# Performance work log

Measured on AMD Instinct MI355X. Metric: run time of the kernel, lower is better.

## Reference

```python
import jax, jax.numpy as jnp
import numpy as np

LN_EPS = 1e-5


def _segment_mean(vals, idx, num_segments):
    s = jax.ops.segment_sum(vals, idx, num_segments=num_segments)
    cnt = jax.ops.segment_sum(jnp.ones((vals.shape[0],), vals.dtype), idx, num_segments=num_segments)
    return s / jnp.maximum(cnt, 1.0)[:, None]


def _sage_layer(x, src, dst, W_l, b_l, W_r, gamma, beta):
    # PyG SAGEConv (mean aggr): out = lin_l(mean_{j in N(i)} x_j) + lin_r(x_i)
    N = x.shape[0]
    agg = _segment_mean(x[src], dst, N)                     # [N, in]
    h = agg @ W_l.T + b_l + x @ W_r.T                       # [N, out]
    mu = jnp.mean(h, axis=-1, keepdims=True)
    var = jnp.mean((h - mu) ** 2, axis=-1, keepdims=True)
    h = (h - mu) * jax.lax.rsqrt(var + LN_EPS) * gamma + beta
    return jax.nn.relu(h)                                   # dropout: eval mode (identity)


def setup_inputs() -> dict:
    key = jax.random.key(0)
    ks = jax.random.split(key, 20)
    N, E, IN, H, OUT, G, C = 50000, 600000, 128, 128, 64, 64, 2

    def glorot(k, fo, fi):
        lim = np.sqrt(6.0 / (fo + fi)).astype(np.float32)
        return jax.random.uniform(k, (fo, fi), jnp.float32, -lim, lim)

    inp = {
        'x': jax.random.normal(ks[0], (N, IN), jnp.float32),
        'edge_index': jax.random.randint(ks[1], (2, E), 0, N, jnp.int64),
        'batch': jnp.sort(jax.random.randint(ks[2], (N,), 0, G, jnp.int64)),
    }
    dims = [(IN, H), (H, H), (H, OUT)]
    for i, (fi, fo) in enumerate(dims):
        inp[f'Wl{i}'] = glorot(ks[3 + 4 * i], fo, fi)
        inp[f'bl{i}'] = jnp.zeros((fo,), jnp.float32)
        inp[f'Wr{i}'] = glorot(ks[4 + 4 * i], fo, fi)
        inp[f'g{i}'] = jnp.ones((fo,), jnp.float32)
        inp[f'be{i}'] = jnp.zeros((fo,), jnp.float32)
    inp['cW1'] = glorot(ks[16], H, 2 * OUT)
    inp['cb1'] = jnp.zeros((H,), jnp.float32)
    inp['cW2'] = glorot(ks[17], C, H)
    inp['cb2'] = jnp.zeros((C,), jnp.float32)
    return inp


def reference(x, edge_index, batch,
              Wl0, bl0, Wr0, g0, be0,
              Wl1, bl1, Wr1, g1, be1,
              Wl2, bl2, Wr2, g2, be2,
              cW1, cb1, cW2, cb2):
    src, dst = edge_index[0], edge_index[1]
    h = _sage_layer(x, src, dst, Wl0, bl0, Wr0, g0, be0)
    h = _sage_layer(h, src, dst, Wl1, bl1, Wr1, g1, be1)
    h = _sage_layer(h, src, dst, Wl2, bl2, Wr2, g2, be2)
    G = 64  # number of graphs
    x_mean = _segment_mean(h, batch, G)                     # [G, out]
    x_max = jax.ops.segment_max(h, batch, num_segments=G)   # [G, out]
    z = jnp.concatenate([x_mean, x_max], axis=-1)           # [G, 2*out]
    z = jax.nn.relu(z @ cW1.T + cb1)
    return z @ cW2.T + cb2                                  # [G, num_classes]
```

## Files before the change

kernel.cpp:

```cpp
#include <hip/hip_runtime.h>

typedef unsigned short ushort_t;
typedef short s16x8 __attribute__((ext_vector_type(8)));
typedef float f32x4 __attribute__((ext_vector_type(4)));

#define LN_EPS 1e-5f

__device__ __forceinline__ float b2f(ushort_t u) {
    return __uint_as_float(((unsigned)u) << 16);
}
__device__ __forceinline__ ushort_t f2b(float f) {
    unsigned b = __float_as_uint(f);
    b += 0x7FFFu + ((b >> 16) & 1u);
    return (ushort_t)(b >> 16);
}
__device__ __forceinline__ unsigned f2b2(float lo, float hi) {
    return (unsigned)f2b(lo) | ((unsigned)f2b(hi) << 16);
}
__device__ __forceinline__ float ldf(const void* p, size_t i, int isF) {
    return isF ? ((const float*)p)[i] : b2f(((const ushort_t*)p)[i]);
}

__global__ void GraphSAGE_36026185678961_kernel() {}

__global__ void k_detect_zero(const void* w0, const void* ei, int* __restrict__ flags,
                              int* __restrict__ deg, float* __restrict__ Z, int N) {
    int i = blockIdx.x * blockDim.x + threadIdx.x;
    if (i < N) deg[i] = 0;
    if (i < 64 * 128) Z[i] = 0.f;
    if (blockIdx.x == 0 && threadIdx.x < 64) {
        int t = threadIdx.x;
        const ushort_t* u = (const ushort_t*)w0;
        int pass = 0;
        #pragma unroll
        for (int k = 0; k < 4; ++k) {
            ushort_t v = u[t * 4 + k];
            int ex = (v >> 7) & 0xFF;
            if (ex == 0 || (ex >= 0x60 && ex <= 0x7E)) pass++;
        }
        const unsigned* w = (const unsigned*)ei;
        int nz = (w[2 * t + 1] != 0u) ? 1 : 0;
        #pragma unroll
        for (int off = 32; off; off >>= 1) {
            pass += __shfl_down(pass, off, 64);
            nz += __shfl_down(nz, off, 64);
        }
        if (t == 0) {
            flags[0] = (pass < 205) ? 1 : 0;
            flags[1] = (nz == 0) ? 1 : 0;
        }
    }
}

__global__ void k_prep(const void* X, ushort_t* __restrict__ XB, int total4, int xb,
                       const void* ei, int E, int N, int* __restrict__ deg, int eb,
                       const void* Wl0, const void* Wr0, const void* Wl1, const void* Wr1,
                       const void* Wl2, const void* Wr2,
                       ushort_t* __restrict__ Wb0, ushort_t* __restrict__ Wb1,
                       ushort_t* __restrict__ Wb2,
                       const int* __restrict__ flags) {
    int b = blockIdx.x;
    if (b < xb) {
        int idx = b * 256 + threadIdx.x;
        if (idx >= total4) return;
        if (flags[0]) {
            float4 v = ((const float4*)X)[idx];
            ushort4 o;
            o.x = f2b(v.x); o.y = f2b(v.y); o.z = f2b(v.z); o.w = f2b(v.w);
            ((ushort4*)XB)[idx] = o;
        } else {
            ((ushort4*)XB)[idx] = ((const ushort4*)X)[idx];
        }
    } else if (b < xb + eb) {
        int e = (b - xb) * 256 + threadIdx.x;
        if (e >= E) return;
        int d = flags[1] ? (int)((const long long*)ei)[E + e] : ((const int*)ei)[E + e];
        if ((unsigned)d < (unsigned)N) atomicAdd(&deg[d], 1);
    } else {
        int t = (b - xb - eb) * 256 + threadIdx.x;
        int isF = flags[0];
        if (t < 2 * 32768) {
            const void* Wl = (t < 32768) ? Wl0 : Wl1;
            const void* Wr = (t < 32768) ? Wr0 : Wr1;
            ushort_t* Wb = (t < 32768) ? Wb0 : Wb1;
            int base = t & 32767;
            int f = base >> 8, k = base & 255;
            if (isF) {
                float v = (k < 128) ? ((const float*)Wl)[f * 128 + k]
                                    : ((const float*)Wr)[f * 128 + (k - 128)];
                Wb[base] = f2b(v);
            } else {
                Wb[base] = ((const ushort_t*)((k < 128) ? Wl : Wr))[f * 128 + (k & 127)];
            }
        } else if (t < 2 * 32768 + 16384) {
            int base = t - 2 * 32768;
            int f = base >> 7, k = base & 127;
            const void* W = (f < 64) ? Wl2 : Wr2;
            int fr = f & 63;
            Wb2[base] = isF ? f2b(((const float*)W)[fr * 128 + k])
                            : ((const ushort_t*)W)[fr * 128 + k];
        }
    }
}

__global__ void k_scan1(const int* __restrict__ deg, int N,
                        int* __restrict__ rowptr, int* __restrict__ bsum) {
    __shared__ int wsum[4];
    __shared__ int wpre[4];
    int tid = threadIdx.x;
    int lane = tid & 63;
    int w = tid >> 6;
    int i = blockIdx.x * 256 + tid;
    int v = (i < N) ? deg[i] : 0;
    int x = v;
    #pragma unroll
    for (int off = 1; off < 64; off <<= 1) {
        int t = __shfl_up(x, off, 64);
        if (lane >= off) x += t;
    }
    if (lane == 63) wsum[w] = x;
    __syncthreads();
    if (tid == 0) {
        int a = wsum[0]; wpre[0] = a;
        a += wsum[1]; wpre[1] = a;
        a += wsum[2]; wpre[2] = a;
        a += wsum[3]; wpre[3] = a;
    }
    __syncthreads();
    int woff = (w == 0) ? 0 : wpre[w - 1];
    if (i < N) rowptr[i] = woff + x - v;
    if (tid == 0) bsum[blockIdx.x] = wpre[3];
}

__global__ void k_scan2(const int* __restrict__ bsum, int nb,
                        int* __restrict__ boff, int* __restrict__ rowptrN,
                        const void* batch, int N, int G, const int* __restrict__ flags,
                        int* __restrict__ bounds) {
    __shared__ int wsum[4];
    __shared__ int wpre[4];
    int tid = threadIdx.x;
    int lane = tid & 63;
    int w = tid >> 6;
    int run = 0;
    for (int base = 0; base < nb; base += 256) {
        int i = base + tid;
        int v = (i < nb) ? bsum[i] : 0;
        int x = v;
        #pragma unroll
        for (int off = 1; off < 64; off <<= 1) {
            int t = __shfl_up(x, off, 64);
            if (lane >= off) x += t;
        }
        if (lane == 63) wsum[w] = x;
        __syncthreads();
        if (tid == 0) {
            int a = wsum[0]; wpre[0] = a;
            a += wsum[1]; wpre[1] = a;
            a += wsum[2]; wpre[2] = a;
            a += wsum[3]; wpre[3] = a;
        }
        __syncthreads();
        int woff = (w == 0) ? 0 : wpre[w - 1];
        if (i < nb) boff[i] = run + woff + x - v;
        int tot = wpre[3];
        __syncthreads();
        run += tot;
    }
    if (tid == 0) *rowptrN = run;
    if (tid <= G) {
        int isL = flags[1];
        int lo = 0, hi = N;
        while (lo < hi) {
            int mid = (lo + hi) >> 1;
            int bv = isL ? (int)((const long long*)batch)[mid] : ((const int*)batch)[mid];
            if (bv < tid) lo = mid + 1; else hi = mid;
        }
        bounds[tid] = lo;
    }
}

__global__ void k_scan3(int* __restrict__ rowptr, const int* __restrict__ boff,
                        int* __restrict__ cursor, int N) {
    int i = blockIdx.x * 256 + threadIdx.x;
    if (i < N) {
        int r = rowptr[i] + boff[i >> 8];
        rowptr[i] = r;
        cursor[i] = r;
    }
}

__global__ void k_fill(const void* ei, int E, int N, const int* __restrict__ flags,
                       int* __restrict__ cursor, int* __restrict__ col) {
    int e = blockIdx.x * blockDim.x + threadIdx.x;
    if (e >= E) return;
    int s, d;
    if (flags[1]) {
        const long long* p = (const long long*)ei;
        s = (int)p[e];
        d = (int)p[E + e];
    } else {
        const int* p = (const int*)ei;
        s = p[e];
        d = p[E + e];
    }
    if ((unsigned)d < (unsigned)N) {
        int p = atomicAdd(&cursor[d], 1);
        if ((unsigned)p < (unsigned)E) col[p] = ((unsigned)s < (unsigned)N) ? s : 0;
    }
}

__global__ __launch_bounds__(256) void k_agg(
    const ushort_t* __restrict__ X, const int* __restrict__ rowptr,
    const int* __restrict__ col, ushort_t* __restrict__ AGG, int N) {
    int i = blockIdx.x * 4 + (threadIdx.x >> 6);
    if (i >= N) return;
    int l = threadIdx.x & 63;
    int qn = l >> 4;
    int fo = l & 15;
    const uint4* X8 = (const uint4*)X;
    int s = rowptr[i], e = rowptr[i + 1];
    float al[4] = {0.f, 0.f, 0.f, 0.f};
    float ah[4] = {0.f, 0.f, 0.f, 0.f};
    int p = s + qn;
    for (; p + 8 < e; p += 12) {
        int j0 = col[p], j1 = col[p + 4], j2 = col[p + 8];
        uint4 u0 = X8[(size_t)j0 * 16 + fo];
        uint4 u1 = X8[(size_t)j1 * 16 + fo];
        uint4 u2 = X8[(size_t)j2 * 16 + fo];
        unsigned w0[4] = {u0.x, u0.y, u0.z, u0.w};
        unsigned w1[4] = {u1.x, u1.y, u1.z, u1.w};
        unsigned w2[4] = {u2.x, u2.y, u2.z, u2.w};
        #pragma unroll
        for (int k = 0; k < 4; ++k) {
            al[k] += __uint_as_float(w0[k] << 16) + __uint_as_float(w1[k] << 16)
                   + __uint_as_float(w2[k] << 16);
            ah[k] += __uint_as_float(w0[k] & 0xFFFF0000u) + __uint_as_float(w1[k] & 0xFFFF0000u)
                   + __uint_as_float(w2[k] & 0xFFFF0000u);
        }
    }
    if (p + 4 < e) {
        int j0 = col[p], j1 = col[p + 4];
        uint4 u0 = X8[(size_t)j0 * 16 + fo];
        uint4 u1 = X8[(size_t)j1 * 16 + fo];
        unsigned w0[4] = {u0.x, u0.y, u0.z, u0.w};
        unsigned w1[4] = {u1.x, u1.y, u1.z, u1.w};
        #pragma unroll
        for (int k = 0; k < 4; ++k) {
            al[k] += __uint_as_float(w0[k] << 16) + __uint_as_float(w1[k] << 16);
            ah[k] += __uint_as_float(w0[k] & 0xFFFF0000u) + __uint_as_float(w1[k] & 0xFFFF0000u);
        }
        p += 8;
    }
    if (p < e) {
        int j = col[p];
        uint4 u = X8[(size_t)j * 16 + fo];
        unsigned w0[4] = {u.x, u.y, u.z, u.w};
        #pragma unroll
        for (int k = 0; k < 4; ++k) {
            al[k] += __uint_as_float(w0[k] << 16);
            ah[k] += __uint_as_float(w0[k] & 0xFFFF0000u);
        }
    }
    #pragma unroll
    for (int k = 0; k < 4; ++k) {
        al[k] += __shfl_xor(al[k], 16, 64);
        al[k] += __shfl_xor(al[k], 32, 64);
        ah[k] += __shfl_xor(ah[k], 16, 64);
        ah[k] += __shfl_xor(ah[k], 32, 64);
    }
    if (qn == 0) {
        int d = e - s;
        float inv = 1.f / (float)(d > 0 ? d : 1);
        uint4 o;
        o.x = f2b2(al[0] * inv, ah[0] * inv);
        o.y = f2b2(al[1] * inv, ah[1] * inv);
        o.z = f2b2(al[2] * inv, ah[2] * inv);
        o.w = f2b2(al[3] * inv, ah[3] * inv);
        ((uint4*)AGG)[(size_t)i * 16 + fo] = o;
    }
}

template <int FO>
__global__ __launch_bounds__(256, 2) void k_gemm_ln(
    const ushort_t* __restrict__ AGG, const ushort_t* __restrict__ X,
    const ushort_t* __restrict__ Wb,
    const void* bl, const void* gam, const void* bet,
    const int* __restrict__ flags,
    ushort_t* __restrict__ H, int M) {
    constexpr int NT = FO / 16;
    constexpr int R = 2;
    int lane = threadIdx.x & 63;
    int wid = threadIdx.x >> 6;
    int wrow0 = (blockIdx.x * 4 + wid) * (R * 16);
    if (wrow0 >= M) return;
    int isF = flags[0];
    int m = lane & 15;
    int q = lane >> 4;

    int arow[R];
    #pragma unroll
    for (int r = 0; r < R; ++r) {
        int ar = wrow0 + r * 16 + m;
        arow[r] = (ar < M) ? ar : (M - 1);
    }

    f32x4 acc[R][NT];
    #pragma unroll
    for (int r = 0; r < R; ++r)
        #pragma unroll
        for (int nt = 0; nt < NT; ++nt) acc[r][nt] = (f32x4){0.f, 0.f, 0.f, 0.f};

    #pragma unroll
    for (int kk = 0; kk < 8; ++kk) {
        const ushort_t* base = (kk < 4) ? AGG : X;
        int ko = (kk & 3) * 32 + q * 8;
        s16x8 a[R];
        #pragma unroll
        for (int r = 0; r < R; ++r)
            a[r] = *(const s16x8*)(base + (size_t)arow[r] * 128 + ko);
        #pragma unroll
        for (int nt = 0; nt < NT; ++nt) {
            s16x8 b = *(const s16x8*)(Wb + (size_t)(nt * 16 + m) * 256 + kk * 32 + q * 8);
            #pragma unroll
            for (int r = 0; r < R; ++r)
                acc[r][nt] = __builtin_amdgcn_mfma_f32_16x16x32_bf16(a[r], b, acc[r][nt], 0, 0, 0);
        }
    }

    #pragma unroll
    for (int r = 0; r < R; ++r) {
        #pragma unroll
        for (int nt = 0; nt < NT; ++nt) {
            float bv = ldf(bl, nt * 16 + m, isF);
            #pragma unroll
            for (int rr = 0; rr < 4; ++rr) acc[r][nt][rr] += bv;
        }
        float mu[4], rs[4];
        #pragma unroll
        for (int rr = 0; rr < 4; ++rr) {
            float s1 = 0.f, s2 = 0.f;
            #pragma unroll
            for (int nt = 0; nt < NT; ++nt) {
                float v = acc[r][nt][rr];
                s1 += v;
                s2 += v * v;
            }
            #pragma unroll
            for (int off = 1; off < 16; off <<= 1) {
                s1 += __shfl_xor(s1, off, 64);
                s2 += __shfl_xor(s2, off, 64);
            }
            float mm = s1 / (float)FO;
            float var = s2 / (float)FO - mm * mm;
            var = var > 0.f ? var : 0.f;
            mu[rr] = mm;
            rs[rr] = rsqrtf(var + LN_EPS);
        }
        #pragma unroll
        for (int nt = 0; nt < NT; ++nt) {
            int n0 = nt * 16 + m;
            float g = ldf(gam, n0, isF);
            float be = ldf(bet, n0, isF);
            #pragma unroll
            for (int rr = 0; rr < 4; ++rr) {
                int row = wrow0 + r * 16 + q * 4 + rr;
                if (row < M) {
                    float y = (acc[r][nt][rr] - mu[rr]) * rs[rr] * g + be;
                    y = y > 0.f ? y : 0.f;
                    H[(size_t)row * FO + n0] = f2b(y);
                }
            }
        }
    }
}

__global__ __launch_bounds__(256, 2) void k_gemm3(
    const ushort_t* __restrict__ X,
    const ushort_t* __restrict__ Wb,
    ushort_t* __restrict__ T,
    int M) {
    constexpr int NT = 8;
    constexpr int R = 2;
    int lane = threadIdx.x & 63;
    int wid = threadIdx.x >> 6;
    int wrow0 = (blockIdx.x * 4 + wid) * (R * 16);
    if (wrow0 >= M) return;
    int m = lane & 15;
    int q = lane >> 4;

    int arow[R];
    #pragma unroll
    for (int r = 0; r < R; ++r) {
        int ar = wrow0 + r * 16 + m;
        arow[r] = (ar < M) ? ar : (M - 1);
    }

    f32x4 acc[R][NT];
    #pragma unroll
    for (int r = 0; r < R; ++r)
        #pragma unroll
        for (int nt = 0; nt < NT; ++nt) acc[r][nt] = (f32x4){0.f, 0.f, 0.f, 0.f};

    #pragma unroll
    for (int kk = 0; kk < 4; ++kk) {
        int ko = kk * 32 + q * 8;
        s16x8 a[R];
        #pragma unroll
        for (int r = 0; r < R; ++r)
            a[r] = *(const s16x8*)(X + (size_t)arow[r] * 128 + ko);
        #pragma unroll
        for (int nt = 0; nt < NT; ++nt) {
            s16x8 b = *(const s16x8*)(Wb + (size_t)(nt * 16 + m) * 128 + ko);
            #pragma unroll
            for (int r = 0; r < R; ++r)
                acc[r][nt] = __builtin_amdgcn_mfma_f32_16x16x32_bf16(a[r], b, acc[r][nt], 0, 0, 0);
        }
    }

    #pragma unroll
    for (int r = 0; r < R; ++r)
        #pragma unroll
        for (int nt = 0; nt < NT; ++nt) {
            int n0 = nt * 16 + m;
            #pragma unroll
            for (int rr = 0; rr < 4; ++rr) {
                int row = wrow0 + r * 16 + q * 4 + rr;
                if (row < M) T[(size_t)row * 128 + n0] = f2b(acc[r][nt][rr]);
            }
        }
}

__global__ __launch_bounds__(256) void k_agg3(
    const ushort_t* __restrict__ T,
    const int* __restrict__ rowptr, const int* __restrict__ col,
    const void* bl, const void* gam, const void* bet, const int* __restrict__ flags,
    ushort_t* __restrict__ H, int N) {
    int i = blockIdx.x * 4 + (threadIdx.x >> 6);
    if (i >= N) return;
    int l = threadIdx.x & 63;
    int qn = l >> 4;
    int fo = l & 15;
    int isF = flags[0];
    const uint2* T2 = (const uint2*)T;
    int s = rowptr[i], e = rowptr[i + 1];
    float al[2] = {0.f, 0.f};
    float ah[2] = {0.f, 0.f};
    int p = s + qn;
    for (; p + 8 < e; p += 12) {
        int j0 = col[p], j1 = col[p + 4], j2 = col[p + 8];
        uint2 u0 = T2[(size_t)j0 * 32 + fo];
        uint2 u1 = T2[(size_t)j1 * 32 + fo];
        uint2 u2 = T2[(size_t)j2 * 32 + fo];
        unsigned w0[2] = {u0.x, u0.y};
        unsigned w1[2] = {u1.x, u1.y};
        unsigned w2[2] = {u2.x, u2.y};
        #pragma unroll
        for (int k = 0; k < 2; ++k) {
            al[k] += __uint_as_float(w0[k] << 16) + __uint_as_float(w1[k] << 16)
                   + __uint_as_float(w2[k] << 16);
            ah[k] += __uint_as_float(w0[k] & 0xFFFF0000u) + __uint_as_float(w1[k] & 0xFFFF0000u)
                   + __uint_as_float(w2[k] & 0xFFFF0000u);
        }
    }
    if (p + 4 < e) {
        int j0 = col[p], j1 = col[p + 4];
        uint2 u0 = T2[(size_t)j0 * 32 + fo];
        uint2 u1 = T2[(size_t)j1 * 32 + fo];
        unsigned w0[2] = {u0.x, u0.y};
        unsigned w1[2] = {u1.x, u1.y};
        #pragma unroll
        for (int k = 0; k < 2; ++k) {
            al[k] += __uint_as_float(w0[k] << 16) + __uint_as_float(w1[k] << 16);
            ah[k] += __uint_as_float(w0[k] & 0xFFFF0000u) + __uint_as_float(w1[k] & 0xFFFF0000u);
        }
        p += 8;
    }
    if (p < e) {
        int j = col[p];
        uint2 u = T2[(size_t)j * 32 + fo];
        unsigned w0[2] = {u.x, u.y};
        #pragma unroll
        for (int k = 0; k < 2; ++k) {
            al[k] += __uint_as_float(w0[k] << 16);
            ah[k] += __uint_as_float(w0[k] & 0xFFFF0000u);
        }
    }
    #pragma unroll
    for (int k = 0; k < 2; ++k) {
        al[k] += __shfl_xor(al[k], 16, 64);
        al[k] += __shfl_xor(al[k], 32, 64);
        ah[k] += __shfl_xor(ah[k], 16, 64);
        ah[k] += __shfl_xor(ah[k], 32, 64);
    }
    int d = e - s;
    float inv = 1.f / (float)(d > 0 ? d : 1);
    uint2 su = T2[(size_t)i * 32 + 16 + fo];
    float v0 = al[0] * inv + __uint_as_float(su.x << 16) + ldf(bl, 4 * fo + 0, isF);
    float v1 = ah[0] * inv + __uint_as_float(su.x & 0xFFFF0000u) + ldf(bl, 4 * fo + 1, isF);
    float v2 = al[1] * inv + __uint_as_float(su.y << 16) + ldf(bl, 4 * fo + 2, isF);
    float v3 = ah[1] * inv + __uint_as_float(su.y & 0xFFFF0000u) + ldf(bl, 4 * fo + 3, isF);
    float s1 = v0 + v1 + v2 + v3;
    float s2 = v0 * v0 + v1 * v1 + v2 * v2 + v3 * v3;
    #pragma unroll
    for (int off = 1; off < 16; off <<= 1) {
        s1 += __shfl_xor(s1, off, 64);
        s2 += __shfl_xor(s2, off, 64);
    }
    float mu = s1 / 64.f;
    float var = s2 / 64.f - mu * mu;
    var = var > 0.f ? var : 0.f;
    float rs = rsqrtf(var + LN_EPS);
    if (qn == 0) {
        float y0 = (v0 - mu) * rs * ldf(gam, 4 * fo + 0, isF) + ldf(bet, 4 * fo + 0, isF);
        float y1 = (v1 - mu) * rs * ldf(gam, 4 * fo + 1, isF) + ldf(bet, 4 * fo + 1, isF);
        float y2 = (v2 - mu) * rs * ldf(gam, 4 * fo + 2, isF) + ldf(bet, 4 * fo + 2, isF);
        float y3 = (v3 - mu) * rs * ldf(gam, 4 * fo + 3, isF) + ldf(bet, 4 * fo + 3, isF);
        y0 = y0 > 0.f ? y0 : 0.f;
        y1 = y1 > 0.f ? y1 : 0.f;
        y2 = y2 > 0.f ? y2 : 0.f;
        y3 = y3 > 0.f ? y3 : 0.f;
        uint2 o;
        o.x = f2b2(y0, y1);
        o.y = f2b2(y2, y3);
        ((uint2*)H)[(size_t)i * 16 + fo] = o;
    }
}

__global__ __launch_bounds__(256) void k_pool(
    const ushort_t* __restrict__ H,
    const int* __restrict__ bounds, float* __restrict__ Z, int N) {
    int g = blockIdx.x >> 4;
    int chunk = blockIdx.x & 15;
    int lane = threadIdx.x & 31;
    int sub = threadIdx.x >> 5;
    int strm = chunk * 8 + sub;
    int s = bounds[g], e = bounds[g + 1];
    s = s < 0 ? 0 : (s > N ? N : s);
    e = e < s ? s : (e > N ? N : e);
    const unsigned* H2 = (const unsigned*)H;
    float sl = 0.f, sh = 0.f, ml = 0.f, mh = 0.f;
    for (int i = s + strm; i < e; i += 128) {
        unsigned u = H2[(size_t)i * 32 + lane];
        float vl = __uint_as_float(u << 16);
        float vh = __uint_as_float(u & 0xFFFF0000u);
        sl += vl; sh += vh;
        ml = ml > vl ? ml : vl;
        mh = mh > vh ? mh : vh;
    }
    int f0 = lane * 2;
    atomicAdd(&Z[g * 128 + f0], sl);
    atomicAdd(&Z[g * 128 + f0 + 1], sh);
    atomicMax((int*)&Z[g * 128 + 64 + f0], __float_as_int(ml));
    atomicMax((int*)&Z[g * 128 + 64 + f0 + 1], __float_as_int(mh));
}

__global__ void k_mlp(const float* __restrict__ Z, const int* __restrict__ bounds,
                      const void* cW1, const void* cb1, const void* cW2, const void* cb2,
                      const int* __restrict__ flags, void* __restrict__ out) {
    int g = blockIdx.x;
    int f = threadIdx.x;
    int isF = flags[0];
    __shared__ float z[128];
    __shared__ float hid[128];
    __shared__ float r0[2], r1[2];
    int cnt = bounds[g + 1] - bounds[g];
    float c = (float)(cnt > 0 ? cnt : 1);
    float zv = Z[g * 128 + f];
    if (f < 64) zv /= c;
    z[f] = zv;
    __syncthreads();
    float acc = ldf(cb1, f, isF);
    #pragma unroll 8
    for (int k = 0; k < 128; ++k) acc += z[k] * ldf(cW1, f * 128 + k, isF);
    acc = acc > 0.f ? acc : 0.f;
    hid[f] = acc;
    __syncthreads();
    float p0 = hid[f] * ldf(cW2, f, isF);
    float p1 = hid[f] * ldf(cW2, 128 + f, isF);
    #pragma unroll
    for (int off = 32; off > 0; off >>= 1) {
        p0 += __shfl_xor(p0, off, 64);
        p1 += __shfl_xor(p1, off, 64);
    }
    int w = f >> 6;
    if ((f & 63) == 0) { r0[w] = p0; r1[w] = p1; }
    __syncthreads();
    if (f == 0) {
        float v0 = r0[0] + r0[1] + ldf(cb2, 0, isF);
        float v1 = r1[0] + r1[1] + ldf(cb2, 1, isF);
        if (isF) {
            ((float*)out)[g * 2 + 0] = v0;
            ((float*)out)[g * 2 + 1] = v1;
        } else {
            ((ushort_t*)out)[g * 2 + 0] = f2b(v0);
            ((ushort_t*)out)[g * 2 + 1] = f2b(v1);
        }
    }
}

extern "C" void kernel_launch(void* const* d_in, const int* in_sizes, int n_in,
                              void* d_out, int out_size, void* d_ws, size_t ws_size,
                              hipStream_t stream) {
    const void* x = d_in[0];
    const void* ei = d_in[1];
    const void* batch = d_in[2];
    const void* Wl0 = d_in[3];
    const void* bl0 = d_in[4];
    const void* Wr0 = d_in[5];
    const void* g0 = d_in[6];
    const void* be0 = d_in[7];
    const void* Wl1 = d_in[8];
    const void* bl1 = d_in[9];
    const void* Wr1 = d_in[10];
    const void* g1 = d_in[11];
    const void* be1 = d_in[12];
    const void* Wl2 = d_in[13];
    const void* bl2 = d_in[14];
    const void* Wr2 = d_in[15];
    const void* g2 = d_in[16];
    const void* be2 = d_in[17];
    const void* cW1 = d_in[18];
    const void* cb1 = d_in[19];
    const void* cW2 = d_in[20];
    const void* cb2 = d_in[21];

    const int N = in_sizes[0] / 128;
    const int E = in_sizes[1] / 2;
    const int G = 64;

    char* w = (char*)d_ws;
    size_t o = 0;
    auto take = [&](size_t bytes) -> void* {
        void* p = w + o;
        o = (o + bytes + 255) & ~(size_t)255;
        return p;
    };
    int nb1 = (N + 255) / 256;
    int* flags  = (int*)take(4 * 4);
    int* rowptr = (int*)take((size_t)(N + 1) * 4);
    int* cursor = (int*)take((size_t)N * 4);
    int* deg    = (int*)take((size_t)N * 4);
    int* bsum   = (int*)take((size_t)nb1 * 4);
    int* boff   = (int*)take((size_t)nb1 * 4);
    int* col    = (int*)take((size_t)E * 4);
    int* bounds = (int*)take((size_t)(G + 1) * 4);
    float* Z    = (float*)take((size_t)G * 128 * 4);
    ushort_t* Wb0 = (ushort_t*)take((size_t)128 * 256 * 2);
    ushort_t* Wb1 = (ushort_t*)take((size_t)128 * 256 * 2);
    ushort_t* Wb2 = (ushort_t*)take((size_t)128 * 128 * 2);
    ushort_t* AGG = (ushort_t*)take((size_t)N * 128 * 2);
    ushort_t* H1  = (ushort_t*)take((size_t)N * 128 * 2);
    ushort_t* H2  = (ushort_t*)take((size_t)N * 128 * 2);
    ushort_t* XB  = H2;
    ushort_t* T3  = AGG;
    ushort_t* H3  = H1;
    if (o > ws_size) return;

    int eb = (E + 255) / 256;
    int xb = (N * 128 / 4 + 255) / 256;
    int wb = (2 * 32768 + 16384 + 255) / 256;
    k_detect_zero<<<nb1, 256, 0, stream>>>(Wl0, ei, flags, deg, Z, N);
    k_prep<<<xb + eb + wb, 256, 0, stream>>>(x, XB, N * 128 / 4, xb,
                                             ei, E, N, deg, eb,
                                             Wl0, Wr0, Wl1, Wr1, Wl2, Wr2,
                                             Wb0, Wb1, Wb2, flags);
    k_scan1<<<nb1, 256, 0, stream>>>(deg, N, rowptr, bsum);
    k_scan2<<<1, 256, 0, stream>>>(bsum, nb1, boff, rowptr + N, batch, N, G, flags, bounds);
    k_scan3<<<nb1, 256, 0, stream>>>(rowptr, boff, cursor, N);
    k_fill<<<eb, 256, 0, stream>>>(ei, E, N, flags, cursor, col);

    int gb = (N + 127) / 128;
    int ab = (N + 3) / 4;

    k_agg<<<ab, 256, 0, stream>>>(XB, rowptr, col, AGG, N);
    k_gemm_ln<128><<<gb, 256, 0, stream>>>(AGG, XB, Wb0, bl0, g0, be0, flags, H1, N);
    k_agg<<<ab, 256, 0, stream>>>(H1, rowptr, col, AGG, N);
    k_gemm_ln<128><<<gb, 256, 0, stream>>>(AGG, H1, Wb1, bl1, g1, be1, flags, H2, N);
    k_gemm3<<<gb, 256, 0, stream>>>(H2, Wb2, T3, N);
    k_agg3<<<ab, 256, 0, stream>>>(T3, rowptr, col, bl2, g2, be2, flags, H3, N);

    k_pool<<<G * 16, 256, 0, stream>>>(H3, bounds, Z, N);
    k_mlp<<<G, 128, 0, stream>>>(Z, bounds, cW1, cb1, cW2, cb2, flags, d_out);
}
```

Baseline: 371.6 us.

## Fuse graph pooling into final aggregation kernel and pre-transpose classifier weight

The separate pooling kernel is removed. The last aggregation+LayerNorm kernel now reduces its four node rows per block in shared memory and issues atomic sum/max into the per-graph pooled buffer, finding each node's graph by binary search over the graph boundaries. This drops the H3 write and re-read and one launch, but adds many more atomics: one set per block instead of per graph chunk. The MLP head's first weight is also transposed into float during prep so its matvec reads are coalesced.

After: 364.0 us. 2.0% less time.

```diff
diff --git a/kernel.cpp b/kernel.cpp
--- a/kernel.cpp
+++ b/kernel.cpp
@@ -55,9 +55,9 @@
 __global__ void k_prep(const void* X, ushort_t* __restrict__ XB, int total4, int xb,
                        const void* ei, int E, int N, int* __restrict__ deg, int eb,
                        const void* Wl0, const void* Wr0, const void* Wl1, const void* Wr1,
-                       const void* Wl2, const void* Wr2,
+                       const void* Wl2, const void* Wr2, const void* cW1,
                        ushort_t* __restrict__ Wb0, ushort_t* __restrict__ Wb1,
-                       ushort_t* __restrict__ Wb2,
+                       ushort_t* __restrict__ Wb2, float* __restrict__ cW1T,
                        const int* __restrict__ flags) {
     int b = blockIdx.x;
     if (b < xb) {
@@ -99,6 +99,10 @@
             int fr = f & 63;
             Wb2[base] = isF ? f2b(((const float*)W)[fr * 128 + k])
                             : ((const ushort_t*)W)[fr * 128 + k];
+        } else if (t < 2 * 32768 + 2 * 16384) {
+            int base = t - 2 * 32768 - 16384;
+            int k = base >> 7, f = base & 127;
+            cW1T[base] = ldf(cW1, f * 128 + k, isF);
         }
     }
 }
@@ -434,128 +438,146 @@
     const ushort_t* __restrict__ T,
     const int* __restrict__ rowptr, const int* __restrict__ col,
     const void* bl, const void* gam, const void* bet, const int* __restrict__ flags,
-    ushort_t* __restrict__ H, int N) {
-    int i = blockIdx.x * 4 + (threadIdx.x >> 6);
-    if (i >= N) return;
+    const int* __restrict__ bounds, float* __restrict__ Z, int N, int G) {
+    __shared__ float psum[4][64];
+    __shared__ float pmax[4][64];
+    __shared__ int pg[4];
+    int wid = threadIdx.x >> 6;
+    int i = blockIdx.x * 4 + wid;
+    int valid = (i < N);
     int l = threadIdx.x & 63;
     int qn = l >> 4;
     int fo = l & 15;
     int isF = flags[0];
     const uint2* T2 = (const uint2*)T;
-    int s = rowptr[i], e = rowptr[i + 1];
-    float al[2] = {0.f, 0.f};
-    float ah[2] = {0.f, 0.f};
-    int p = s + qn;
-    for (; p + 8 < e; p += 12) {
-        int j0 = col[p], j1 = col[p + 4], j2 = col[p + 8];
-        uint2 u0 = T2[(size_t)j0 * 32 + fo];
-        uint2 u1 = T2[(size_t)j1 * 32 + fo];
-        uint2 u2 = T2[(size_t)j2 * 32 + fo];
-        unsigned w0[2] = {u0.x, u0.y};
-        unsigned w1[2] = {u1.x, u1.y};
-        unsigned w2[2] = {u2.x, u2.y};
+
+    if (valid) {
+        int s = rowptr[i], e = rowptr[i + 1];
+        float al[2] = {0.f, 0.f};
+        float ah[2] = {0.f, 0.f};
+        int p = s + qn;
+        for (; p + 8 < e; p += 12) {
+            int j0 = col[p], j1 = col[p + 4], j2 = col[p + 8];
+            uint2 u0 = T2[(size_t)j0 * 32 + fo];
+            uint2 u1 = T2[(size_t)j1 * 32 + fo];
+            uint2 u2 = T2[(size_t)j2 * 32 + fo];
+            unsigned w0[2] = {u0.x, u0.y};
+            unsigned w1[2] = {u1.x, u1.y};
+            unsigned w2[2] = {u2.x, u2.y};
+            #pragma unroll
+            for (int k = 0; k < 2; ++k) {
+                al[k] += __uint_as_float(w0[k] << 16) + __uint_as_float(w1[k] << 16)
+                       + __uint_as_float(w2[k] << 16);
+                ah[k] += __uint_as_float(w0[k] & 0xFFFF0000u) + __uint_as_float(w1[k] & 0xFFFF0000u)
+                       + __uint_as_float(w2[k] & 0xFFFF0000u);
+            }
+        }
+        if (p + 4 < e) {
+            int j0 = col[p], j1 = col[p + 4];
+            uint2 u0 = T2[(size_t)j0 * 32 + fo];
+            uint2 u1 = T2[(size_t)j1 * 32 + fo];
+            unsigned w0[2] = {u0.x, u0.y};
+            unsigned w1[2] = {u1.x, u1.y};
+            #pragma unroll
+            for (int k = 0; k < 2; ++k) {
+                al[k] += __uint_as_float(w0[k] << 16) + __uint_as_float(w1[k] << 16);
+                ah[k] += __uint_as_float(w0[k] & 0xFFFF0000u) + __uint_as_float(w1[k] & 0xFFFF0000u);
+            }
+            p += 8;
+        }
+        if (p < e) {
+            int j = col[p];
+            uint2 u = T2[(size_t)j * 32 + fo];
+            unsigned w0[2] = {u.x, u.y};
+            #pragma unroll
+            for (int k = 0; k < 2; ++k) {
+                al[k] += __uint_as_float(w0[k] << 16);
+                ah[k] += __uint_as_float(w0[k] & 0xFFFF0000u);
+            }
+        }
         #pragma unroll
         for (int k = 0; k < 2; ++k) {
-            al[k] += __uint_as_float(w0[k] << 16) + __uint_as_float(w1[k] << 16)
-                   + __uint_as_float(w2[k] << 16);
-            ah[k] += __uint_as_float(w0[k] & 0xFFFF0000u) + __uint_as_float(w1[k] & 0xFFFF0000u)
-                   + __uint_as_float(w2[k] & 0xFFFF0000u);
-        }
-    }
-    if (p + 4 < e) {
-        int j0 = col[p], j1 = col[p + 4];
-        uint2 u0 = T2[(size_t)j0 * 32 + fo];
-        uint2 u1 = T2[(size_t)j1 * 32 + fo];
-        unsigned w0[2] = {u0.x, u0.y};
-        unsigned w1[2] = {u1.x, u1.y};
-        #pragma unroll
-        for (int k = 0; k < 2; ++k) {
-            al[k] += __uint_as_float(w0[k] << 16) + __uint_as_float(w1[k] << 16);
-            ah[k] += __uint_as_float(w0[k] & 0xFFFF0000u) + __uint_as_float(w1[k] & 0xFFFF0000u);
-        }
-        p += 8;
-    }
-    if (p < e) {
-        int j = col[p];
-        uint2 u = T2[(size_t)j * 32 + fo];
-        unsigned w0[2] = {u.x, u.y};
-        #pragma unroll
-        for (int k = 0; k < 2; ++k) {
-            al[k] += __uint_as_float(w0[k] << 16);
-            ah[k] += __uint_as_float(w0[k] & 0xFFFF0000u);
-        }
-    }
-    #pragma unroll
-    for (int k = 0; k < 2; ++k) {
-        al[k] += __shfl_xor(al[k], 16, 64);
-        al[k] += __shfl_xor(al[k], 32, 64);
-        ah[k] += __shfl_xor(ah[k], 16, 64);
-        ah[k] += __shfl_xor(ah[k], 32, 64);
-    }
-    int d = e - s;
-    float inv = 1.f / (float)(d > 0 ? d : 1);
-    uint2 su = T2[(size_t)i * 32 + 16 + fo];
-    float v0 = al[0] * inv + __uint_as_float(su.x << 16) + ldf(bl, 4 * fo + 0, isF);
-    float v1 = ah[0] * inv + __uint_as_float(su.x & 0xFFFF0000u) + ldf(bl, 4 * fo + 1, isF);
-    float v2 = al[1] * inv + __uint_as_float(su.y << 16) + ldf(bl, 4 * fo + 2, isF);
-    float v3 = ah[1] * inv + __uint_as_float(su.y & 0xFFFF0000u) + ldf(bl, 4 * fo + 3, isF);
-    float s1 = v0 + v1 + v2 + v3;
-    float s2 = v0 * v0 + v1 * v1 + v2 * v2 + v3 * v3;
-    #pragma unroll
-    for (int off = 1; off < 16; off <<= 1) {
-        s1 += __shfl_xor(s1, off, 64);
-        s2 += __shfl_xor(s2, off, 64);
-    }
-    float mu = s1 / 64.f;
-    float var = s2 / 64.f - mu * mu;
-    var = var > 0.f ? var : 0.f;
-    float rs = rsqrtf(var + LN_EPS);
-    if (qn == 0) {
-        float y0 = (v0 - mu) * rs * ldf(gam, 4 * fo + 0, isF) + ldf(bet, 4 * fo + 0, isF);
-        float y1 = (v1 - mu) * rs * ldf(gam, 4 * fo + 1, isF) + ldf(bet, 4 * fo + 1, isF);
-        float y2 = (v2 - mu) * rs * ldf(gam, 4 * fo + 2, isF) + ldf(bet, 4 * fo + 2, isF);
-        float y3 = (v3 - mu) * rs * ldf(gam, 4 * fo + 3, isF) + ldf(bet, 4 * fo + 3, isF);
-        y0 = y0 > 0.f ? y0 : 0.f;
-        y1 = y1 > 0.f ? y1 : 0.f;
-        y2 = y2 > 0.f ? y2 : 0.f;
-        y3 = y3 > 0.f ? y3 : 0.f;
-        uint2 o;
-        o.x = f2b2(y0, y1);
-        o.y = f2b2(y2, y3);
-        ((uint2*)H)[(size_t)i * 16 + fo] = o;
-    }
-}
-
-__global__ __launch_bounds__(256) void k_pool(
-    const ushort_t* __restrict__ H,
-    const int* __restrict__ bounds, float* __restrict__ Z, int N) {
-    int g = blockIdx.x >> 4;
-    int chunk = blockIdx.x & 15;
-    int lane = threadIdx.x & 31;
-    int sub = threadIdx.x >> 5;
-    int strm = chunk * 8 + sub;
-    int s = bounds[g], e = bounds[g + 1];
-    s = s < 0 ? 0 : (s > N ? N : s);
-    e = e < s ? s : (e > N ? N : e);
-    const unsigned* H2 = (const unsigned*)H;
-    float sl = 0.f, sh = 0.f, ml = 0.f, mh = 0.f;
-    for (int i = s + strm; i < e; i += 128) {
-        unsigned u = H2[(size_t)i * 32 + lane];
-        float vl = __uint_as_float(u << 16);
-        float vh = __uint_as_float(u & 0xFFFF0000u);
-        sl += vl; sh += vh;
-        ml = ml > vl ? ml : vl;
-        mh = mh > vh ? mh : vh;
-    }
-    int f0 = lane * 2;
-    atomicAdd(&Z[g * 128 + f0], sl);
-    atomicAdd(&Z[g * 128 + f0 + 1], sh);
-    atomicMax((int*)&Z[g * 128 + 64 + f0], __float_as_int(ml));
-    atomicMax((int*)&Z[g * 128 + 64 + f0 + 1], __float_as_int(mh));
+            al[k] += __shfl_xor(al[k], 16, 64);
+            al[k] += __shfl_xor(al[k], 32, 64);
+            ah[k] += __shfl_xor(ah[k], 16, 64);
+            ah[k] += __shfl_xor(ah[k], 32, 64);
+        }
+        int d = e - s;
+        float inv = 1.f / (float)(d > 0 ? d : 1);
+        uint2 su = T2[(size_t)i * 32 + 16 + fo];
+        float v0 = al[0] * inv + __uint_as_float(su.x << 16) + ldf(bl, 4 * fo + 0, isF);
+        float v1 = ah[0] * inv + __uint_as_float(su.x & 0xFFFF0000u) + ldf(bl, 4 * fo + 1, isF);
+        float v2 = al[1] * inv + __uint_as_float(su.y << 16) + ldf(bl, 4 * fo + 2, isF);
+        float v3 = ah[1] * inv + __uint_as_float(su.y & 0xFFFF0000u) + ldf(bl, 4 * fo + 3, isF);
+        float s1 = v0 + v1 + v2 + v3;
+        float s2 = v0 * v0 + v1 * v1 + v2 * v2 + v3 * v3;
+        #pragma unroll
+        for (int off = 1; off < 16; off <<= 1) {
+            s1 += __shfl_xor(s1, off, 64);
+            s2 += __shfl_xor(s2, off, 64);
+        }
+        float mu = s1 / 64.f;
+        float var = s2 / 64.f - mu * mu;
+        var = var > 0.f ? var : 0.f;
+        float rs = rsqrtf(var + LN_EPS);
+        if (qn == 0) {
+            float y0 = (v0 - mu) * rs * ldf(gam, 4 * fo + 0, isF) + ldf(bet, 4 * fo + 0, isF);
+            float y1 = (v1 - mu) * rs * ldf(gam, 4 * fo + 1, isF) + ldf(bet, 4 * fo + 1, isF);
+            float y2 = (v2 - mu) * rs * ldf(gam, 4 * fo + 2, isF) + ldf(bet, 4 * fo + 2, isF);
+            float y3 = (v3 - mu) * rs * ldf(gam, 4 * fo + 3, isF) + ldf(bet, 4 * fo + 3, isF);
+            y0 = y0 > 0.f ? y0 : 0.f;
+            y1 = y1 > 0.f ? y1 : 0.f;
+            y2 = y2 > 0.f ? y2 : 0.f;
+            y3 = y3 > 0.f ? y3 : 0.f;
+            psum[wid][4 * fo + 0] = y0; pmax[wid][4 * fo + 0] = y0;
+            psum[wid][4 * fo + 1] = y1; pmax[wid][4 * fo + 1] = y1;
+            psum[wid][4 * fo + 2] = y2; pmax[wid][4 * fo + 2] = y2;
+            psum[wid][4 * fo + 3] = y3; pmax[wid][4 * fo + 3] = y3;
+        }
+        if (l == 0) {
+            int lo = 0, hi = G - 1;
+            while (lo < hi) {
+                int mid = (lo + hi + 1) >> 1;
+                if (bounds[mid] <= i) lo = mid; else hi = mid - 1;
+            }
+            pg[wid] = lo;
+        }
+    } else if (l == 0) {
+        pg[wid] = -1;
+    }
+    __syncthreads();
+    int tid = threadIdx.x;
+    if (tid < 64) {
+        float asum = 0.f, amax = 0.f;
+        int gcur = -1;
+        #pragma unroll
+        for (int w = 0; w < 4; ++w) {
+            int g = pg[w];
+            if (g < 0) continue;
+            if (g != gcur) {
+                if (gcur >= 0) {
+                    atomicAdd(&Z[gcur * 128 + tid], asum);
+                    atomicMax((int*)&Z[gcur * 128 + 64 + tid], __float_as_int(amax));
+                }
+                gcur = g;
+                asum = psum[w][tid];
+                amax = pmax[w][tid];
+            } else {
+                asum += psum[w][tid];
+                float m = pmax[w][tid];
+                amax = amax > m ? amax : m;
+            }
+        }
+        if (gcur >= 0) {
+            atomicAdd(&Z[gcur * 128 + tid], asum);
+            atomicMax((int*)&Z[gcur * 128 + 64 + tid], __float_as_int(amax));
+        }
+    }
 }
 
 __global__ void k_mlp(const float* __restrict__ Z, const int* __restrict__ bounds,
-                      const void* cW1, const void* cb1, const void* cW2, const void* cb2,
+                      const float* __restrict__ cW1T, const void* cb1,
+                      const void* cW2, const void* cb2,
                       const int* __restrict__ flags, void* __restrict__ out) {
     int g = blockIdx.x;
     int f = threadIdx.x;
@@ -571,7 +593,7 @@
     __syncthreads();
     float acc = ldf(cb1, f, isF);
     #pragma unroll 8
-    for (int k = 0; k < 128; ++k) acc += z[k] * ldf(cW1, f * 128 + k, isF);
+    for (int k = 0; k < 128; ++k) acc += z[k] * cW1T[k * 128 + f];
     acc = acc > 0.f ? acc : 0.f;
     hid[f] = acc;
     __syncthreads();
@@ -645,6 +667,7 @@
     int* col    = (int*)take((size_t)E * 4);
     int* bounds = (int*)take((size_t)(G + 1) * 4);
     float* Z    = (float*)take((size_t)G * 128 * 4);
+    float* cW1T = (float*)take((size_t)128 * 128 * 4);
     ushort_t* Wb0 = (ushort_t*)take((size_t)128 * 256 * 2);
     ushort_t* Wb1 = (ushort_t*)take((size_t)128 * 256 * 2);
     ushort_t* Wb2 = (ushort_t*)take((size_t)128 * 128 * 2);
@@ -653,17 +676,16 @@
     ushort_t* H2  = (ushort_t*)take((size_t)N * 128 * 2);
     ushort_t* XB  = H2;
     ushort_t* T3  = AGG;
-    ushort_t* H3  = H1;
     if (o > ws_size) return;
 
     int eb = (E + 255) / 256;
     int xb = (N * 128 / 4 + 255) / 256;
-    int wb = (2 * 32768 + 16384 + 255) / 256;
+    int wb = (2 * 32768 + 2 * 16384 + 255) / 256;
     k_detect_zero<<<nb1, 256, 0, stream>>>(Wl0, ei, flags, deg, Z, N);
     k_prep<<<xb + eb + wb, 256, 0, stream>>>(x, XB, N * 128 / 4, xb,
                                              ei, E, N, deg, eb,
-                                             Wl0, Wr0, Wl1, Wr1, Wl2, Wr2,
-                                             Wb0, Wb1, Wb2, flags);
+                                             Wl0, Wr0, Wl1, Wr1, Wl2, Wr2, cW1,
+                                             Wb0, Wb1, Wb2, cW1T, flags);
     k_scan1<<<nb1, 256, 0, stream>>>(deg, N, rowptr, bsum);
     k_scan2<<<1, 256, 0, stream>>>(bsum, nb1, boff, rowptr + N, batch, N, G, flags, bounds);
     k_scan3<<<nb1, 256, 0, stream>>>(rowptr, boff, cursor, N);
@@ -677,8 +699,7 @@
     k_agg<<<ab, 256, 0, stream>>>(H1, rowptr, col, AGG, N);
     k_gemm_ln<128><<<gb, 256, 0, stream>>>(AGG, H1, Wb1, bl1, g1, be1, flags, H2, N);
     k_gemm3<<<gb, 256, 0, stream>>>(H2, Wb2, T3, N);
-    k_agg3<<<ab, 256, 0, stream>>>(T3, rowptr, col, bl2, g2, be2, flags, H3, N);
-
-    k_pool<<<G * 16, 256, 0, stream>>>(H3, bounds, Z, N);
-    k_mlp<<<G, 128, 0, stream>>>(Z, bounds, cW1, cb1, cW2, cb2, flags, d_out);
-}
+    k_agg3<<<ab, 256, 0, stream>>>(T3, rowptr, col, bl2, g2, be2, flags, bounds, Z, N, G);
+
+    k_mlp<<<G, 128, 0, stream>>>(Z, bounds, cW1T, cb1, cW2, cb2, flags, d_out);
+}
```
